# Kernel optimization log

Measured on AMD Instinct MI355X. Metric: run time of the kernel, lower is better.

Reference implementation:

```python
import jax, jax.numpy as jnp
import numpy as np

B, L, D, H = 4, 2048, 1024, 8
DH = D // H
NEG = float(-2**32 + 1)  # padding value used by the torch module


def setup_inputs() -> dict:
    key = jax.random.key(0)
    ks = jax.random.split(key, 7)
    queries = jax.random.normal(ks[0], (B, L, D), dtype=jnp.float32)
    keys = jax.random.normal(ks[1], (B, L, D), dtype=jnp.float32)
    sequence_length = jax.random.randint(ks[2], (B,), 1, L + 1, dtype=jnp.int32)
    scale = 0.02
    W_q = jax.random.normal(ks[3], (D, D), dtype=jnp.float32) * scale
    W_k = jax.random.normal(ks[4], (D, D), dtype=jnp.float32) * scale
    W_v = jax.random.normal(ks[5], (D, D), dtype=jnp.float32) * scale
    W_o = jax.random.normal(ks[6], (D, D), dtype=jnp.float32) * scale
    return {"queries": queries, "keys": keys, "sequence_length": sequence_length,
            "W_q": W_q, "W_k": W_k, "W_v": W_v, "W_o": W_o}


def reference(queries, keys, sequence_length, W_q, W_k, W_v, W_o):
    b, lq, d = queries.shape
    lk = keys.shape[1]
    # projections (nn.Linear, no bias): x @ W.T
    Q = (queries @ W_q.T).reshape(b, lq, H, DH).transpose(2, 0, 1, 3)  # (H,B,Lq,dh)
    K = (keys @ W_k.T).reshape(b, lk, H, DH).transpose(2, 0, 1, 3)
    V = (keys @ W_v.T).reshape(b, lk, H, DH).transpose(2, 0, 1, 3)
    scores = jnp.einsum('hbqd,hbkd->hbqk', Q, K) / jnp.sqrt(jnp.float32(DH))
    # additive key mask: positions >= sequence_length get large negative
    key_mask = jnp.arange(lk)[None, :] < sequence_length[:, None]      # (B,Lk)
    scores = jnp.where(key_mask[None, :, None, :], scores, NEG)
    attn = jax.nn.softmax(scores, axis=-1)
    # post-softmax multiplicative query mask
    q_mask = (jnp.arange(lq)[None, :] < sequence_length[:, None]).astype(attn.dtype)  # (B,Lq)
    attn = attn * q_mask[None, :, :, None]
    out = jnp.einsum('hbqk,hbkd->hbqd', attn, V)                       # (H,B,Lq,dh)
    # chunk-cat order: head h occupies columns h*dh:(h+1)*dh
    out = out.transpose(1, 2, 0, 3).reshape(b, lq, d)
    return out @ W_o.T  # dropout_rate=0 -> identity
```

## Files before the change

kernel.cpp:

```cpp
#include <hip/hip_runtime.h>
#include <math.h>

constexpr int Bsz = 4;
constexpr int Lsz = 2048;
constexpr int Dsz = 1024;
constexpr int Hn  = 8;
constexpr int Dh  = 128;
constexpr int GM  = Bsz * Lsz;
constexpr int GK  = Dsz;
constexpr int NT  = GK / 32;

typedef __attribute__((ext_vector_type(8))) short bf16x8;
typedef __attribute__((ext_vector_type(4))) float f32x4;

union FragU { unsigned int u[4]; bf16x8 f; };

__device__ __forceinline__ void gload16(const void* g, void* l) {
    __builtin_amdgcn_global_load_lds(
        (const __attribute__((address_space(1))) unsigned int*)g,
        (__attribute__((address_space(3))) unsigned int*)l, 16, 0, 0);
}

__device__ __forceinline__ void split2(float f0, float f1,
                                       unsigned int& hp, unsigned int& lp) {
    unsigned int u0 = __float_as_uint(f0), u1 = __float_as_uint(f1);
    hp = (u0 >> 16) | (u1 & 0xffff0000u);
    float l0 = f0 - __uint_as_float(u0 & 0xffff0000u);
    float l1 = f1 - __uint_as_float(u1 & 0xffff0000u);
    lp = (__float_as_uint(l0) >> 16) | (__float_as_uint(l1) & 0xffff0000u);
}

__device__ __forceinline__ void split4(float4 f, ushort4& h, ushort4& l2) {
    unsigned int ux = __float_as_uint(f.x), uy = __float_as_uint(f.y),
                 uz = __float_as_uint(f.z), uw = __float_as_uint(f.w);
    h.x = (unsigned short)(ux >> 16); h.y = (unsigned short)(uy >> 16);
    h.z = (unsigned short)(uz >> 16); h.w = (unsigned short)(uw >> 16);
    float lx = f.x - __uint_as_float(ux & 0xffff0000u);
    float ly = f.y - __uint_as_float(uy & 0xffff0000u);
    float lz = f.z - __uint_as_float(uz & 0xffff0000u);
    float lw = f.w - __uint_as_float(uw & 0xffff0000u);
    l2.x = (unsigned short)(__float_as_uint(lx) >> 16);
    l2.y = (unsigned short)(__float_as_uint(ly) >> 16);
    l2.z = (unsigned short)(__float_as_uint(lz) >> 16);
    l2.w = (unsigned short)(__float_as_uint(lw) >> 16);
}

struct WConv4 {
    const float4* w[4];
    ushort4* h[4];
    ushort4* l[4];
    float s[4];
};

__global__ __launch_bounds__(256) void conv_w4(WConv4 a) {
    int wi = blockIdx.x >> 10;
    int i = (blockIdx.x & 1023) * 256 + threadIdx.x;
    float4 f = a.w[wi][i];
    float s = a.s[wi];
    f.x *= s; f.y *= s; f.z *= s; f.w *= s;
    ushort4 h, l;
    split4(f, h, l);
    a.h[wi][i] = h; a.l[wi][i] = l;
}

__device__ __forceinline__ void compute_tile(const ushort* Ah, const ushort* Al,
                                             const ushort* Bh, const ushort* Bl,
                                             int wm, int wn, int l,
                                             f32x4 acc[2][4]) {
    bf16x8 bh[4], bl4[4], ah[2], al[2];
#pragma unroll
    for (int fn = 0; fn < 4; ++fn) {
        int fng = wn * 4 + fn;
        bh[fn]  = *(const bf16x8*)&Bh[(fng * 64 + l) * 8];
        bl4[fn] = *(const bf16x8*)&Bl[(fng * 64 + l) * 8];
    }
#pragma unroll
    for (int fm = 0; fm < 2; ++fm) {
        int fmg = wm * 2 + fm;
        ah[fm] = *(const bf16x8*)&Ah[(fmg * 64 + l) * 8];
        al[fm] = *(const bf16x8*)&Al[(fmg * 64 + l) * 8];
    }
    __builtin_amdgcn_s_setprio(1);
#pragma unroll
    for (int fm = 0; fm < 2; ++fm)
#pragma unroll
        for (int fn = 0; fn < 4; ++fn) {
            acc[fm][fn] = __builtin_amdgcn_mfma_f32_16x16x32_bf16(
                ah[fm], bh[fn], acc[fm][fn], 0, 0, 0);
            acc[fm][fn] = __builtin_amdgcn_mfma_f32_16x16x32_bf16(
                ah[fm], bl4[fn], acc[fm][fn], 0, 0, 0);
            acc[fm][fn] = __builtin_amdgcn_mfma_f32_16x16x32_bf16(
                al[fm], bh[fn], acc[fm][fn], 0, 0, 0);
        }
    __builtin_amdgcn_s_setprio(0);
}

__device__ __forceinline__ void split_write(ushort* Ah, ushort* Al, int aw,
                                            float4 v0, float4 v1) {
    uint4 h4, l4;
    split2(v0.x, v0.y, h4.x, l4.x);
    split2(v0.z, v0.w, h4.y, l4.y);
    split2(v1.x, v1.y, h4.z, l4.z);
    split2(v1.z, v1.w, h4.w, l4.w);
    *(uint4*)&Ah[aw] = h4;
    *(uint4*)&Al[aw] = l4;
}

__global__ __launch_bounds__(512, 2) void gemm_qkv(
    const float* __restrict__ Aq, const float* __restrict__ Ak,
    const ushort* __restrict__ Wfh, const ushort* __restrict__ Wfl,
    ushort* __restrict__ Qhi, ushort* __restrict__ Qlo,
    ushort* __restrict__ Khi, ushort* __restrict__ Klo,
    ushort* __restrict__ Vthi, ushort* __restrict__ Vtlo,
    const int* __restrict__ slen)
{
    const int tid = threadIdx.x;
    const int bm = blockIdx.y << 7;
    const int bn = blockIdx.x << 7;
    const int grp = bn >> 10;

    const int nk = slen[bm >> 11];
    if ((bm & (Lsz - 1)) >= nk) return;

    __shared__ __align__(16) ushort lds[2][4][128 * 32];

    const float* A = (grp == 0) ? Aq : Ak;
    const int w  = tid >> 6;
    const int l  = tid & 63;
    const int wm = w >> 1;
    const int wn = w & 1;

    const int arow = tid >> 2;
    const int akk  = (tid & 3) << 3;
    const float* ag = A + (size_t)(bm + arow) * GK + akk;
    const int aw = ((((arow >> 4) << 6) + ((akk >> 3) << 4) + (arow & 15)) << 3);

    const int brow = ((tid >> 6) << 4) + (tid & 15);
    const int bkk  = ((tid >> 4) & 3) << 3;
    const ushort* bgh = Wfh + (size_t)(bn + brow) * GK + bkk;
    const ushort* bgl = Wfl + (size_t)(bn + brow) * GK + bkk;

    f32x4 acc[2][4];
#pragma unroll
    for (int i = 0; i < 2; ++i)
#pragma unroll
        for (int j = 0; j < 4; ++j) acc[i][j] = (f32x4)0.f;

    {
        float4 tC0 = *(const float4*)(ag);
        float4 tC1 = *(const float4*)(ag + 4);
        gload16(bgh, &lds[0][2][tid * 8]);
        gload16(bgl, &lds[0][3][tid * 8]);
        split_write(&lds[0][0][0], &lds[0][1][0], aw, tC0, tC1);
    }
    float4 rN0 = *(const float4*)(ag + 32);
    float4 rN1 = *(const float4*)(ag + 36);
    float4 rA0, rA1;
    __syncthreads();

    for (int t = 0; t < NT - 2; t += 2) {
        rA0 = *(const float4*)(ag + (t + 2) * 32);
        rA1 = *(const float4*)(ag + (t + 2) * 32 + 4);
        gload16(bgh + (t + 1) * 32, &lds[1][2][tid * 8]);
        gload16(bgl + (t + 1) * 32, &lds[1][3][tid * 8]);
        split_write(&lds[1][0][0], &lds[1][1][0], aw, rN0, rN1);
        compute_tile(&lds[0][0][0], &lds[0][1][0], &lds[0][2][0], &lds[0][3][0],
                     wm, wn, l, acc);
        __syncthreads();

        rN0 = *(const float4*)(ag + (t + 3) * 32);
        rN1 = *(const float4*)(ag + (t + 3) * 32 + 4);
        gload16(bgh + (t + 2) * 32, &lds[0][2][tid * 8]);
        gload16(bgl + (t + 2) * 32, &lds[0][3][tid * 8]);
        split_write(&lds[0][0][0], &lds[0][1][0], aw, rA0, rA1);
        compute_tile(&lds[1][0][0], &lds[1][1][0], &lds[1][2][0], &lds[1][3][0],
                     wm, wn, l, acc);
        __syncthreads();
    }

    gload16(bgh + (NT - 1) * 32, &lds[1][2][tid * 8]);
    gload16(bgl + (NT - 1) * 32, &lds[1][3][tid * 8]);
    split_write(&lds[1][0][0], &lds[1][1][0], aw, rN0, rN1);
    compute_tile(&lds[0][0][0], &lds[0][1][0], &lds[0][2][0], &lds[0][3][0],
                 wm, wn, l, acc);
    __syncthreads();

    compute_tile(&lds[1][0][0], &lds[1][1][0], &lds[1][2][0], &lds[1][3][0],
                 wm, wn, l, acc);

    const int rq = (l >> 4) << 2;
    const int cq = l & 15;
    ushort* OH = (grp == 0) ? Qhi : Khi;
    ushort* OL = (grp == 0) ? Qlo : Klo;
#pragma unroll
    for (int fm = 0; fm < 2; ++fm) {
        int r0 = bm + wm * 32 + fm * 16 + rq;
#pragma unroll
        for (int fn = 0; fn < 4; ++fn) {
            int cn = (bn & 1023) + wn * 64 + fn * 16 + cq;
            if (grp < 2) {
#pragma unroll
                for (int r = 0; r < 4; ++r) {
                    float f = acc[fm][fn][r];
                    unsigned int u = __float_as_uint(f);
                    float res = f - __uint_as_float(u & 0xffff0000u);
                    OH[(size_t)(r0 + r) * Dsz + cn] = (unsigned short)(u >> 16);
                    OL[(size_t)(r0 + r) * Dsz + cn] =
                        (unsigned short)(__float_as_uint(res) >> 16);
                }
            } else {
                ushort4 h4, l4;
                unsigned short* hp = (unsigned short*)&h4;
                unsigned short* lp = (unsigned short*)&l4;
#pragma unroll
                for (int r = 0; r < 4; ++r) {
                    float f = acc[fm][fn][r];
                    unsigned int u = __float_as_uint(f);
                    float res = f - __uint_as_float(u & 0xffff0000u);
                    hp[r] = (unsigned short)(u >> 16);
                    lp[r] = (unsigned short)(__float_as_uint(res) >> 16);
                }
                *(ushort4*)&Vthi[(size_t)cn * GM + r0] = h4;
                *(ushort4*)&Vtlo[(size_t)cn * GM + r0] = l4;
            }
        }
    }
}

__global__ __launch_bounds__(512, 2) void gemm_o(
    const ushort* __restrict__ Ahi, const ushort* __restrict__ Alo,
    const ushort* __restrict__ Bhi, const ushort* __restrict__ Blo,
    float* __restrict__ C, const int* __restrict__ slen)
{
    const int tid = threadIdx.x;
    const int bm = blockIdx.y << 7;
    const int bn = blockIdx.x << 7;

    const int nk = slen[bm >> 11];
    if ((bm & (Lsz - 1)) >= nk) {
        int row = tid >> 2;
        int cb  = (tid & 3) << 5;
        float4 z = make_float4(0.f, 0.f, 0.f, 0.f);
        float4* cp = (float4*)(C + (size_t)(bm + row) * Dsz + bn + cb);
#pragma unroll
        for (int i = 0; i < 8; ++i) cp[i] = z;
        return;
    }

    __shared__ __align__(16) ushort lds[2][4][128 * 32];

    const int w  = tid >> 6;
    const int l  = tid & 63;
    const int wm = w >> 1;
    const int wn = w & 1;

    const int srow = ((tid >> 6) << 4) + (tid & 15);
    const int skk  = ((tid >> 4) & 3) << 3;
    const ushort* agh = Ahi + (size_t)(bm + srow) * GK + skk;
    const ushort* agl = Alo + (size_t)(bm + srow) * GK + skk;
    const ushort* bgh = Bhi + (size_t)(bn + srow) * GK + skk;
    const ushort* bgl = Blo + (size_t)(bn + srow) * GK + skk;

    f32x4 acc[2][4];
#pragma unroll
    for (int i = 0; i < 2; ++i)
#pragma unroll
        for (int j = 0; j < 4; ++j) acc[i][j] = (f32x4)0.f;

    gload16(agh, &lds[0][0][tid * 8]);
    gload16(agl, &lds[0][1][tid * 8]);
    gload16(bgh, &lds[0][2][tid * 8]);
    gload16(bgl, &lds[0][3][tid * 8]);
    __syncthreads();

    for (int t = 0; t < NT - 1; ++t) {
        const int p = t & 1;
        const int q = p ^ 1;
        gload16(agh + (t + 1) * 32, &lds[q][0][tid * 8]);
        gload16(agl + (t + 1) * 32, &lds[q][1][tid * 8]);
        gload16(bgh + (t + 1) * 32, &lds[q][2][tid * 8]);
        gload16(bgl + (t + 1) * 32, &lds[q][3][tid * 8]);
        compute_tile(&lds[p][0][0], &lds[p][1][0], &lds[p][2][0], &lds[p][3][0],
                     wm, wn, l, acc);
        __syncthreads();
    }
    {
        const int p = (NT - 1) & 1;
        compute_tile(&lds[p][0][0], &lds[p][1][0], &lds[p][2][0], &lds[p][3][0],
                     wm, wn, l, acc);
    }

    const int rq = (l >> 4) << 2;
    const int cq = l & 15;
#pragma unroll
    for (int fm = 0; fm < 2; ++fm) {
        int r0 = bm + wm * 32 + fm * 16 + rq;
#pragma unroll
        for (int fn = 0; fn < 4; ++fn) {
            int c0 = bn + wn * 64 + fn * 16 + cq;
#pragma unroll
            for (int r = 0; r < 4; ++r)
                C[(size_t)(r0 + r) * Dsz + c0] = acc[fm][fn][r];
        }
    }
}

__global__ __launch_bounds__(512) void flash_mfma(
    const ushort* __restrict__ Qhi, const ushort* __restrict__ Qlo,
    const ushort* __restrict__ Khi, const ushort* __restrict__ Klo,
    const ushort* __restrict__ Vthi, const ushort* __restrict__ Vtlo,
    const int* __restrict__ slen,
    ushort* __restrict__ Ohi, ushort* __restrict__ Olo)
{
    __shared__ __align__(16) ushort Ks[32 * 256];
    __shared__ __align__(16) ushort Vs[128 * 64];
    __shared__ __align__(16) unsigned int Pb[8 * 16 * 36];

    const int tid = threadIdx.x;
    const int w = tid >> 6, l = tid & 63;
    const int lg = l >> 4, lc = l & 15;
    const int q0 = blockIdx.x << 7;
    const int h = blockIdx.y, b = blockIdx.z;
    const int nk = slen[b];

    if (q0 >= nk) return;

    bf16x8 qh[4], ql[4];
    {
        size_t base = (size_t)(b * Lsz + q0 + (w << 4) + lc) * Dsz + h * Dh + lg * 8;
#pragma unroll
        for (int s = 0; s < 4; ++s) {
            qh[s] = *(const bf16x8*)&Qhi[base + s * 32];
            ql[s] = *(const bf16x8*)&Qlo[base + s * 32];
        }
    }

    const ushort* ksrc[2]; int klds[2];
    const ushort* vsrc[2]; int vlds[2];
#pragma unroll
    for (int i = 0; i < 2; ++i) {
        int s = i * 512 + tid;
        int j = s >> 5, p = s & 31;
        int lg4 = (p & 15) ^ (j & 15);
        const ushort* base = (p & 16) ? Klo : Khi;
        ksrc[i] = base + (size_t)(b * Lsz + j) * Dsz + h * Dh + lg4 * 8;
        klds[i] = s * 8;
    }
#pragma unroll
    for (int i = 0; i < 2; ++i) {
        int s = i * 512 + tid;
        int d = s >> 3, p = s & 7;
        int lgc = p ^ (d & 7);
        const ushort* base = (lgc & 4) ? Vtlo : Vthi;
        vsrc[i] = base + (size_t)(h * Dh + d) * (Bsz * Lsz) + b * Lsz + (lgc & 3) * 8;
        vlds[i] = s * 8;
    }

    f32x4 oacc[8];
#pragma unroll
    for (int fd = 0; fd < 8; ++fd) oacc[fd] = (f32x4)0.f;
    float lsum[4] = {0.f, 0.f, 0.f, 0.f};
    const int pbase = w * (16 * 36);

    for (int kb = 0; kb < nk; kb += 32) {
#pragma unroll
        for (int i = 0; i < 2; ++i) gload16(ksrc[i] + (size_t)kb * Dsz, &Ks[klds[i]]);
#pragma unroll
        for (int i = 0; i < 2; ++i) gload16(vsrc[i] + kb, &Vs[vlds[i]]);
        __syncthreads();

        f32x4 sa[2] = {(f32x4)0.f, (f32x4)0.f};
#pragma unroll
        for (int fn = 0; fn < 2; ++fn) {
            int j = fn * 16 + lc;
            int ro = j * 256;
#pragma unroll
            for (int s = 0; s < 4; ++s) {
                int phys = (s * 4 + lg) ^ (j & 15);
                bf16x8 kh = *(const bf16x8*)&Ks[ro + phys * 8];
                bf16x8 kl = *(const bf16x8*)&Ks[ro + 128 + phys * 8];
                sa[fn] = __builtin_amdgcn_mfma_f32_16x16x32_bf16(qh[s], kh, sa[fn], 0, 0, 0);
                sa[fn] = __builtin_amdgcn_mfma_f32_16x16x32_bf16(qh[s], kl, sa[fn], 0, 0, 0);
                sa[fn] = __builtin_amdgcn_mfma_f32_16x16x32_bf16(ql[s], kh, sa[fn], 0, 0, 0);
            }
        }

        if (kb + 32 > nk) {
#pragma unroll
            for (int fn = 0; fn < 2; ++fn) {
                bool oob = (kb + fn * 16 + lc) >= nk;
#pragma unroll
                for (int rr = 0; rr < 4; ++rr)
                    sa[fn][rr] = oob ? -1e30f : sa[fn][rr];
            }
        }

#pragma unroll
        for (int fn = 0; fn < 2; ++fn)
#pragma unroll
            for (int rr = 0; rr < 4; ++rr) {
                float p = __expf(sa[fn][rr]);
                lsum[rr] += p;
                unsigned int u = __float_as_uint(p);
                float res = p - __uint_as_float(u & 0xffff0000u);
                unsigned int lo16 = __float_as_uint(res) >> 16;
                Pb[pbase + (lg * 4 + rr) * 36 + fn * 16 + lc] =
                    (lo16 << 16) | (u >> 16);
            }

        const unsigned int* pr = &Pb[pbase + lc * 36 + lg * 8];
        uint4 a0 = *(const uint4*)pr;
        uint4 a1 = *(const uint4*)(pr + 4);
        FragU PH, PL;
        PH.u[0] = (a0.x & 0xffffu) | (a0.y << 16);
        PH.u[1] = (a0.z & 0xffffu) | (a0.w << 16);
        PH.u[2] = (a1.x & 0xffffu) | (a1.y << 16);
        PH.u[3] = (a1.z & 0xffffu) | (a1.w << 16);
        PL.u[0] = (a0.x >> 16) | (a0.y & 0xffff0000u);
        PL.u[1] = (a0.z >> 16) | (a0.w & 0xffff0000u);
        PL.u[2] = (a1.x >> 16) | (a1.y & 0xffff0000u);
        PL.u[3] = (a1.z >> 16) | (a1.w & 0xffff0000u);

#pragma unroll
        for (int fd = 0; fd < 8; ++fd) {
            int d = fd * 16 + lc;
            int ro = d * 64;
            int ph = lg ^ (d & 7);
            int pl2 = (4 + lg) ^ (d & 7);
            bf16x8 vh = *(const bf16x8*)&Vs[ro + ph * 8];
            bf16x8 vl = *(const bf16x8*)&Vs[ro + pl2 * 8];
            oacc[fd] = __builtin_amdgcn_mfma_f32_16x16x32_bf16(PH.f, vh, oacc[fd], 0, 0, 0);
            oacc[fd] = __builtin_amdgcn_mfma_f32_16x16x32_bf16(PH.f, vl, oacc[fd], 0, 0, 0);
            oacc[fd] = __builtin_amdgcn_mfma_f32_16x16x32_bf16(PL.f, vh, oacc[fd], 0, 0, 0);
        }
        __syncthreads();
    }

#pragma unroll
    for (int m = 1; m < 16; m <<= 1)
#pragma unroll
        for (int rr = 0; rr < 4; ++rr)
            lsum[rr] += __shfl_xor(lsum[rr], m, 64);

#pragma unroll
    for (int rr = 0; rr < 4; ++rr) {
        int q = q0 + (w << 4) + (lg << 2) + rr;
        bool valid = q < nk;
        float inv = valid ? (1.f / lsum[rr]) : 0.f;
        size_t base = (size_t)(b * Lsz + q) * Dsz + h * Dh + lc;
#pragma unroll
        for (int fd = 0; fd < 8; ++fd) {
            float val = valid ? oacc[fd][rr] * inv : 0.f;
            unsigned int u = __float_as_uint(val);
            float res = val - __uint_as_float(u & 0xffff0000u);
            Ohi[base + fd * 16] = (unsigned short)(u >> 16);
            Olo[base + fd * 16] = (unsigned short)(__float_as_uint(res) >> 16);
        }
    }
}

extern "C" void kernel_launch(void* const* d_in, const int* in_sizes, int n_in,
                              void* d_out, int out_size, void* d_ws, size_t ws_size,
                              hipStream_t stream) {
    (void)in_sizes; (void)n_in; (void)out_size; (void)ws_size;
    const float* queries = (const float*)d_in[0];
    const float* keys    = (const float*)d_in[1];
    const int*   slen    = (const int*)d_in[2];
    const float* Wq      = (const float*)d_in[3];
    const float* Wk      = (const float*)d_in[4];
    const float* Wv      = (const float*)d_in[5];
    const float* Wo      = (const float*)d_in[6];
    float* out = (float*)d_out;

    const size_t MD = (size_t)Bsz * Lsz * Dsz;
    const size_t WD = (size_t)Dsz * Dsz;
    ushort* Qhi  = (ushort*)d_ws;
    ushort* Qlo  = Qhi + MD;
    ushort* Khi  = Qlo + MD;
    ushort* Klo  = Khi + MD;
    ushort* Vthi = Klo + MD;
    ushort* Vtlo = Vthi + MD;
    ushort* Wfh  = Vtlo + MD;
    ushort* Wfl  = Wfh + 3 * WD;
    ushort* Woh  = Wfl + 3 * WD;
    ushort* Wol  = Woh + WD;

    const float scaleQ = 0.08838834764831845f;
    WConv4 wa;
    wa.w[0] = (const float4*)Wq; wa.h[0] = (ushort4*)Wfh;            wa.l[0] = (ushort4*)Wfl;            wa.s[0] = scaleQ;
    wa.w[1] = (const float4*)Wk; wa.h[1] = (ushort4*)(Wfh + WD);     wa.l[1] = (ushort4*)(Wfl + WD);     wa.s[1] = 1.f;
    wa.w[2] = (const float4*)Wv; wa.h[2] = (ushort4*)(Wfh + 2 * WD); wa.l[2] = (ushort4*)(Wfl + 2 * WD); wa.s[2] = 1.f;
    wa.w[3] = (const float4*)Wo; wa.h[3] = (ushort4*)Woh;            wa.l[3] = (ushort4*)Wol;            wa.s[3] = 1.f;
    conv_w4<<<4096, 256, 0, stream>>>(wa);

    gemm_qkv<<<dim3(24, 64), 512, 0, stream>>>(
        queries, keys, Wfh, Wfl, Qhi, Qlo, Khi, Klo, Vthi, Vtlo, slen);

    dim3 ga(Lsz / 128, Hn, Bsz);
    flash_mfma<<<ga, 512, 0, stream>>>(Qhi, Qlo, Khi, Klo, Vthi, Vtlo, slen,
                                       Qhi, Qlo );

    gemm_o<<<dim3(8, 64), 512, 0, stream>>>(Qhi, Qlo, Woh, Wol, out, slen);
}
```

Before: 395.0 us.

## Use partial vmcnt waits and XOR-swizzle A tile LDS layout in GEMMs

The GEMM main loops now wait for only the older global-to-LDS loads (vmcnt 4/2/0) before a raw barrier, instead of a full __syncthreads, so the next tile's loads stay in flight while the current tile computes. The QKV GEMM also XOR-swizzles the row index of the A tile in LDS to reduce bank conflicts on the split-bf16 writes and reads. The hand-written waitcnt values depend on exact instruction counts and could race if the compiler emits a different number of memory operations.

```diff
diff --git a/kernel.cpp b/kernel.cpp
--- a/kernel.cpp
+++ b/kernel.cpp
@@ -65,7 +65,7 @@
 
 __device__ __forceinline__ void compute_tile(const ushort* Ah, const ushort* Al,
                                              const ushort* Bh, const ushort* Bl,
-                                             int wm, int wn, int l,
+                                             int wm, int wn, int l, int la,
                                              f32x4 acc[2][4]) {
     bf16x8 bh[4], bl4[4], ah[2], al[2];
 #pragma unroll
@@ -77,8 +77,8 @@
 #pragma unroll
     for (int fm = 0; fm < 2; ++fm) {
         int fmg = wm * 2 + fm;
-        ah[fm] = *(const bf16x8*)&Ah[(fmg * 64 + l) * 8];
-        al[fm] = *(const bf16x8*)&Al[(fmg * 64 + l) * 8];
+        ah[fm] = *(const bf16x8*)&Ah[(fmg * 64 + la) * 8];
+        al[fm] = *(const bf16x8*)&Al[(fmg * 64 + la) * 8];
     }
     __builtin_amdgcn_s_setprio(1);
 #pragma unroll
@@ -105,6 +105,19 @@
     *(uint4*)&Ah[aw] = h4;
     *(uint4*)&Al[aw] = l4;
 }
+
+#define FRONT_WAIT_4()  do { \
+    asm volatile("s_waitcnt vmcnt(4) lgkmcnt(0)" ::: "memory"); \
+    __builtin_amdgcn_sched_barrier(0); \
+    __builtin_amdgcn_s_barrier(); } while (0)
+#define FRONT_WAIT_2()  do { \
+    asm volatile("s_waitcnt vmcnt(2) lgkmcnt(0)" ::: "memory"); \
+    __builtin_amdgcn_sched_barrier(0); \
+    __builtin_amdgcn_s_barrier(); } while (0)
+#define FRONT_WAIT_0()  do { \
+    asm volatile("s_waitcnt vmcnt(0) lgkmcnt(0)" ::: "memory"); \
+    __builtin_amdgcn_sched_barrier(0); \
+    __builtin_amdgcn_s_barrier(); } while (0)
 
 __global__ __launch_bounds__(512, 2) void gemm_qkv(
     const float* __restrict__ Aq, const float* __restrict__ Ak,
@@ -129,11 +142,12 @@
     const int l  = tid & 63;
     const int wm = w >> 1;
     const int wn = w & 1;
+    const int la = l ^ ((l >> 4) << 1);
 
     const int arow = tid >> 2;
-    const int akk  = (tid & 3) << 3;
-    const float* ag = A + (size_t)(bm + arow) * GK + akk;
-    const int aw = ((((arow >> 4) << 6) + ((akk >> 3) << 4) + (arow & 15)) << 3);
+    const int kg   = tid & 3;
+    const float* ag = A + (size_t)(bm + arow) * GK + (kg << 3);
+    const int aw = ((((arow >> 4) << 6) + (kg << 4) + ((arow & 15) ^ (kg << 1))) << 3);
 
     const int brow = ((tid >> 6) << 4) + (tid & 15);
     const int bkk  = ((tid >> 4) & 3) << 3;
@@ -146,47 +160,48 @@
 #pragma unroll
         for (int j = 0; j < 4; ++j) acc[i][j] = (f32x4)0.f;
 
-    {
-        float4 tC0 = *(const float4*)(ag);
-        float4 tC1 = *(const float4*)(ag + 4);
-        gload16(bgh, &lds[0][2][tid * 8]);
-        gload16(bgl, &lds[0][3][tid * 8]);
-        split_write(&lds[0][0][0], &lds[0][1][0], aw, tC0, tC1);
-    }
-    float4 rN0 = *(const float4*)(ag + 32);
-    float4 rN1 = *(const float4*)(ag + 36);
-    float4 rA0, rA1;
-    __syncthreads();
+    float4 pA0 = *(const float4*)(ag);
+    float4 pA1 = *(const float4*)(ag + 4);
+    gload16(bgh, &lds[0][2][tid * 8]);
+    gload16(bgl, &lds[0][3][tid * 8]);
+    float4 rA0 = *(const float4*)(ag + 32);
+    float4 rA1 = *(const float4*)(ag + 36);
+    float4 rB0, rB1;
+    split_write(&lds[0][0][0], &lds[0][1][0], aw, pA0, pA1);
 
     for (int t = 0; t < NT - 2; t += 2) {
-        rA0 = *(const float4*)(ag + (t + 2) * 32);
-        rA1 = *(const float4*)(ag + (t + 2) * 32 + 4);
+        rB0 = *(const float4*)(ag + (t + 2) * 32);
+        rB1 = *(const float4*)(ag + (t + 2) * 32 + 4);
         gload16(bgh + (t + 1) * 32, &lds[1][2][tid * 8]);
         gload16(bgl + (t + 1) * 32, &lds[1][3][tid * 8]);
-        split_write(&lds[1][0][0], &lds[1][1][0], aw, rN0, rN1);
+        split_write(&lds[1][0][0], &lds[1][1][0], aw, rA0, rA1);
+        FRONT_WAIT_4();
         compute_tile(&lds[0][0][0], &lds[0][1][0], &lds[0][2][0], &lds[0][3][0],
-                     wm, wn, l, acc);
-        __syncthreads();
-
-        rN0 = *(const float4*)(ag + (t + 3) * 32);
-        rN1 = *(const float4*)(ag + (t + 3) * 32 + 4);
+                     wm, wn, l, la, acc);
+        __builtin_amdgcn_s_barrier();
+
+        rA0 = *(const float4*)(ag + (t + 3) * 32);
+        rA1 = *(const float4*)(ag + (t + 3) * 32 + 4);
         gload16(bgh + (t + 2) * 32, &lds[0][2][tid * 8]);
         gload16(bgl + (t + 2) * 32, &lds[0][3][tid * 8]);
-        split_write(&lds[0][0][0], &lds[0][1][0], aw, rA0, rA1);
+        split_write(&lds[0][0][0], &lds[0][1][0], aw, rB0, rB1);
+        FRONT_WAIT_4();
         compute_tile(&lds[1][0][0], &lds[1][1][0], &lds[1][2][0], &lds[1][3][0],
-                     wm, wn, l, acc);
-        __syncthreads();
+                     wm, wn, l, la, acc);
+        __builtin_amdgcn_s_barrier();
     }
 
     gload16(bgh + (NT - 1) * 32, &lds[1][2][tid * 8]);
     gload16(bgl + (NT - 1) * 32, &lds[1][3][tid * 8]);
-    split_write(&lds[1][0][0], &lds[1][1][0], aw, rN0, rN1);
+    split_write(&lds[1][0][0], &lds[1][1][0], aw, rA0, rA1);
+    FRONT_WAIT_2();
     compute_tile(&lds[0][0][0], &lds[0][1][0], &lds[0][2][0], &lds[0][3][0],
-                 wm, wn, l, acc);
-    __syncthreads();
-
+                 wm, wn, l, la, acc);
+    __builtin_amdgcn_s_barrier();
+
+    FRONT_WAIT_0();
     compute_tile(&lds[1][0][0], &lds[1][1][0], &lds[1][2][0], &lds[1][3][0],
-                 wm, wn, l, acc);
+                 wm, wn, l, la, acc);
 
     const int rq = (l >> 4) << 2;
     const int cq = l & 15;
@@ -267,28 +282,35 @@
 #pragma unroll
         for (int j = 0; j < 4; ++j) acc[i][j] = (f32x4)0.f;
 
-    gload16(agh, &lds[0][0][tid * 8]);
-    gload16(agl, &lds[0][1][tid * 8]);
-    gload16(bgh, &lds[0][2][tid * 8]);
-    gload16(bgl, &lds[0][3][tid * 8]);
-    __syncthreads();
-
-    for (int t = 0; t < NT - 1; ++t) {
-        const int p = t & 1;
-        const int q = p ^ 1;
-        gload16(agh + (t + 1) * 32, &lds[q][0][tid * 8]);
-        gload16(agl + (t + 1) * 32, &lds[q][1][tid * 8]);
-        gload16(bgh + (t + 1) * 32, &lds[q][2][tid * 8]);
-        gload16(bgl + (t + 1) * 32, &lds[q][3][tid * 8]);
-        compute_tile(&lds[p][0][0], &lds[p][1][0], &lds[p][2][0], &lds[p][3][0],
-                     wm, wn, l, acc);
-        __syncthreads();
-    }
-    {
-        const int p = (NT - 1) & 1;
-        compute_tile(&lds[p][0][0], &lds[p][1][0], &lds[p][2][0], &lds[p][3][0],
-                     wm, wn, l, acc);
-    }
+#define STAGE_O(tt, bb) do { \
+    gload16(agh + (tt) * 32, &lds[bb][0][tid * 8]); \
+    gload16(agl + (tt) * 32, &lds[bb][1][tid * 8]); \
+    gload16(bgh + (tt) * 32, &lds[bb][2][tid * 8]); \
+    gload16(bgl + (tt) * 32, &lds[bb][3][tid * 8]); } while (0)
+
+    STAGE_O(0, 0);
+
+    for (int t = 0; t < NT - 2; t += 2) {
+        STAGE_O(t + 1, 1);
+        FRONT_WAIT_4();
+        compute_tile(&lds[0][0][0], &lds[0][1][0], &lds[0][2][0], &lds[0][3][0],
+                     wm, wn, l, l, acc);
+        __builtin_amdgcn_s_barrier();
+        STAGE_O(t + 2, 0);
+        FRONT_WAIT_4();
+        compute_tile(&lds[1][0][0], &lds[1][1][0], &lds[1][2][0], &lds[1][3][0],
+                     wm, wn, l, l, acc);
+        __builtin_amdgcn_s_barrier();
+    }
+    STAGE_O(NT - 1, 1);
+    FRONT_WAIT_4();
+    compute_tile(&lds[0][0][0], &lds[0][1][0], &lds[0][2][0], &lds[0][3][0],
+                 wm, wn, l, l, acc);
+    __builtin_amdgcn_s_barrier();
+    FRONT_WAIT_0();
+    compute_tile(&lds[1][0][0], &lds[1][1][0], &lds[1][2][0], &lds[1][3][0],
+                 wm, wn, l, l, acc);
+#undef STAGE_O
 
     const int rq = (l >> 4) << 2;
     const int cq = l & 15;
```

New measurement: 399.8 us. Within noise of the previous version (+1.2%).

## Load A fragments directly into registers, stage only B through LDS in projection GEMMs

Applied to the files above, without the earlier changes.

In both the QKV and output projection GEMMs, the A operand is now read from global memory straight into each wave's MFMA fragment registers, with the hi/lo bf16 split done in registers, rather than being staged through shared memory. Only the weight (B) tiles keep going through double-buffered LDS, so the LDS footprint halves and launch bounds rise to allow more resident blocks. The aim is to cut LDS writes, LDS reads and footprint per block. The cost is that each wave re-reads its A rows from global memory, because waves sharing the same rows no longer share them through LDS.

```diff
diff --git a/kernel.cpp b/kernel.cpp
--- a/kernel.cpp
+++ b/kernel.cpp
@@ -28,6 +28,13 @@
     float l0 = f0 - __uint_as_float(u0 & 0xffff0000u);
     float l1 = f1 - __uint_as_float(u1 & 0xffff0000u);
     lp = (__float_as_uint(l0) >> 16) | (__float_as_uint(l1) & 0xffff0000u);
+}
+
+__device__ __forceinline__ void splitA(float4 f0, float4 f1, FragU& h, FragU& lo) {
+    split2(f0.x, f0.y, h.u[0], lo.u[0]);
+    split2(f0.z, f0.w, h.u[1], lo.u[1]);
+    split2(f1.x, f1.y, h.u[2], lo.u[2]);
+    split2(f1.z, f1.w, h.u[3], lo.u[3]);
 }
 
 __device__ __forceinline__ void split4(float4 f, ushort4& h, ushort4& l2) {
@@ -63,50 +70,31 @@
     a.h[wi][i] = h; a.l[wi][i] = l;
 }
 
-__device__ __forceinline__ void compute_tile(const ushort* Ah, const ushort* Al,
+__device__ __forceinline__ void mfma_cluster(bf16x8 a0h, bf16x8 a0l,
+                                             bf16x8 a1h, bf16x8 a1l,
                                              const ushort* Bh, const ushort* Bl,
-                                             int wm, int wn, int l,
-                                             f32x4 acc[2][4]) {
-    bf16x8 bh[4], bl4[4], ah[2], al[2];
+                                             int wn, int l, f32x4 acc[2][4]) {
+    bf16x8 bh[4], bl4[4];
 #pragma unroll
     for (int fn = 0; fn < 4; ++fn) {
         int fng = wn * 4 + fn;
         bh[fn]  = *(const bf16x8*)&Bh[(fng * 64 + l) * 8];
         bl4[fn] = *(const bf16x8*)&Bl[(fng * 64 + l) * 8];
     }
-#pragma unroll
-    for (int fm = 0; fm < 2; ++fm) {
-        int fmg = wm * 2 + fm;
-        ah[fm] = *(const bf16x8*)&Ah[(fmg * 64 + l) * 8];
-        al[fm] = *(const bf16x8*)&Al[(fmg * 64 + l) * 8];
-    }
     __builtin_amdgcn_s_setprio(1);
 #pragma unroll
-    for (int fm = 0; fm < 2; ++fm)
-#pragma unroll
-        for (int fn = 0; fn < 4; ++fn) {
-            acc[fm][fn] = __builtin_amdgcn_mfma_f32_16x16x32_bf16(
-                ah[fm], bh[fn], acc[fm][fn], 0, 0, 0);
-            acc[fm][fn] = __builtin_amdgcn_mfma_f32_16x16x32_bf16(
-                ah[fm], bl4[fn], acc[fm][fn], 0, 0, 0);
-            acc[fm][fn] = __builtin_amdgcn_mfma_f32_16x16x32_bf16(
-                al[fm], bh[fn], acc[fm][fn], 0, 0, 0);
-        }
+    for (int fn = 0; fn < 4; ++fn) {
+        acc[0][fn] = __builtin_amdgcn_mfma_f32_16x16x32_bf16(a0h, bh[fn],  acc[0][fn], 0, 0, 0);
+        acc[0][fn] = __builtin_amdgcn_mfma_f32_16x16x32_bf16(a0h, bl4[fn], acc[0][fn], 0, 0, 0);
+        acc[0][fn] = __builtin_amdgcn_mfma_f32_16x16x32_bf16(a0l, bh[fn],  acc[0][fn], 0, 0, 0);
+        acc[1][fn] = __builtin_amdgcn_mfma_f32_16x16x32_bf16(a1h, bh[fn],  acc[1][fn], 0, 0, 0);
+        acc[1][fn] = __builtin_amdgcn_mfma_f32_16x16x32_bf16(a1h, bl4[fn], acc[1][fn], 0, 0, 0);
+        acc[1][fn] = __builtin_amdgcn_mfma_f32_16x16x32_bf16(a1l, bh[fn],  acc[1][fn], 0, 0, 0);
+    }
     __builtin_amdgcn_s_setprio(0);
 }
 
-__device__ __forceinline__ void split_write(ushort* Ah, ushort* Al, int aw,
-                                            float4 v0, float4 v1) {
-    uint4 h4, l4;
-    split2(v0.x, v0.y, h4.x, l4.x);
-    split2(v0.z, v0.w, h4.y, l4.y);
-    split2(v1.x, v1.y, h4.z, l4.z);
-    split2(v1.z, v1.w, h4.w, l4.w);
-    *(uint4*)&Ah[aw] = h4;
-    *(uint4*)&Al[aw] = l4;
-}
-
-__global__ __launch_bounds__(512, 2) void gemm_qkv(
+__global__ __launch_bounds__(512, 4) void gemm_qkv(
     const float* __restrict__ Aq, const float* __restrict__ Ak,
     const ushort* __restrict__ Wfh, const ushort* __restrict__ Wfl,
     ushort* __restrict__ Qhi, ushort* __restrict__ Qlo,
@@ -122,18 +110,17 @@
     const int nk = slen[bm >> 11];
     if ((bm & (Lsz - 1)) >= nk) return;
 
-    __shared__ __align__(16) ushort lds[2][4][128 * 32];
+    __shared__ __align__(16) ushort Bs[2][2][128 * 32];
 
     const float* A = (grp == 0) ? Aq : Ak;
     const int w  = tid >> 6;
     const int l  = tid & 63;
     const int wm = w >> 1;
     const int wn = w & 1;
-
-    const int arow = tid >> 2;
-    const int akk  = (tid & 3) << 3;
-    const float* ag = A + (size_t)(bm + arow) * GK + akk;
-    const int aw = ((((arow >> 4) << 6) + ((akk >> 3) << 4) + (arow & 15)) << 3);
+    const int lg = l >> 4, lc = l & 15;
+
+    const float* agA0 = A + (size_t)(bm + wm * 32 +  0 + lc) * GK + lg * 8;
+    const float* agA1 = A + (size_t)(bm + wm * 32 + 16 + lc) * GK + lg * 8;
 
     const int brow = ((tid >> 6) << 4) + (tid & 15);
     const int bkk  = ((tid >> 4) & 3) << 3;
@@ -146,47 +133,68 @@
 #pragma unroll
         for (int j = 0; j < 4; ++j) acc[i][j] = (f32x4)0.f;
 
+    float4 c00 = *(const float4*)(agA0);
+    float4 c01 = *(const float4*)(agA0 + 4);
+    float4 c10 = *(const float4*)(agA1);
+    float4 c11 = *(const float4*)(agA1 + 4);
+    gload16(bgh, &Bs[0][0][tid * 8]);
+    gload16(bgl, &Bs[0][1][tid * 8]);
+    float4 n00 = *(const float4*)(agA0 + 32);
+    float4 n01 = *(const float4*)(agA0 + 36);
+    float4 n10 = *(const float4*)(agA1 + 32);
+    float4 n11 = *(const float4*)(agA1 + 36);
+    __syncthreads();
+
+    for (int t = 0; t < NT - 2; t += 2) {
+        gload16(bgh + (t + 1) * 32, &Bs[1][0][tid * 8]);
+        gload16(bgl + (t + 1) * 32, &Bs[1][1][tid * 8]);
+        {
+            FragU a0h, a0l, a1h, a1l;
+            splitA(c00, c01, a0h, a0l);
+            splitA(c10, c11, a1h, a1l);
+            c00 = *(const float4*)(agA0 + (t + 2) * 32);
+            c01 = *(const float4*)(agA0 + (t + 2) * 32 + 4);
+            c10 = *(const float4*)(agA1 + (t + 2) * 32);
+            c11 = *(const float4*)(agA1 + (t + 2) * 32 + 4);
+            mfma_cluster(a0h.f, a0l.f, a1h.f, a1l.f,
+                         &Bs[0][0][0], &Bs[0][1][0], wn, l, acc);
+        }
+        __syncthreads();
+
+        gload16(bgh + (t + 2) * 32, &Bs[0][0][tid * 8]);
+        gload16(bgl + (t + 2) * 32, &Bs[0][1][tid * 8]);
+        {
+            FragU a0h, a0l, a1h, a1l;
+            splitA(n00, n01, a0h, a0l);
+            splitA(n10, n11, a1h, a1l);
+            n00 = *(const float4*)(agA0 + (t + 3) * 32);
+            n01 = *(const float4*)(agA0 + (t + 3) * 32 + 4);
+            n10 = *(const float4*)(agA1 + (t + 3) * 32);
+            n11 = *(const float4*)(agA1 + (t + 3) * 32 + 4);
+            mfma_cluster(a0h.f, a0l.f, a1h.f, a1l.f,
+                         &Bs[1][0][0], &Bs[1][1][0], wn, l, acc);
+        }
+        __syncthreads();
+    }
+
+    gload16(bgh + (NT - 1) * 32, &Bs[1][0][tid * 8]);
+    gload16(bgl + (NT - 1) * 32, &Bs[1][1][tid * 8]);
     {
-        float4 tC0 = *(const float4*)(ag);
-        float4 tC1 = *(const float4*)(ag + 4);
-        gload16(bgh, &lds[0][2][tid * 8]);
-        gload16(bgl, &lds[0][3][tid * 8]);
-        split_write(&lds[0][0][0], &lds[0][1][0], aw, tC0, tC1);
-    }
-    float4 rN0 = *(const float4*)(ag + 32);
-    float4 rN1 = *(const float4*)(ag + 36);
-    float4 rA0, rA1;
+        FragU a0h, a0l, a1h, a1l;
+        splitA(c00, c01, a0h, a0l);
+        splitA(c10, c11, a1h, a1l);
+        mfma_cluster(a0h.f, a0l.f, a1h.f, a1l.f,
+                     &Bs[0][0][0], &Bs[0][1][0], wn, l, acc);
+    }
     __syncthreads();
 
-    for (int t = 0; t < NT - 2; t += 2) {
-        rA0 = *(const float4*)(ag + (t + 2) * 32);
-        rA1 = *(const float4*)(ag + (t + 2) * 32 + 4);
-        gload16(bgh + (t + 1) * 32, &lds[1][2][tid * 8]);
-        gload16(bgl + (t + 1) * 32, &lds[1][3][tid * 8]);
-        split_write(&lds[1][0][0], &lds[1][1][0], aw, rN0, rN1);
-        compute_tile(&lds[0][0][0], &lds[0][1][0], &lds[0][2][0], &lds[0][3][0],
-                     wm, wn, l, acc);
-        __syncthreads();
-
-        rN0 = *(const float4*)(ag + (t + 3) * 32);
-        rN1 = *(const float4*)(ag + (t + 3) * 32 + 4);
-        gload16(bgh + (t + 2) * 32, &lds[0][2][tid * 8]);
-        gload16(bgl + (t + 2) * 32, &lds[0][3][tid * 8]);
-        split_write(&lds[0][0][0], &lds[0][1][0], aw, rA0, rA1);
-        compute_tile(&lds[1][0][0], &lds[1][1][0], &lds[1][2][0], &lds[1][3][0],
-                     wm, wn, l, acc);
-        __syncthreads();
-    }
-
-    gload16(bgh + (NT - 1) * 32, &lds[1][2][tid * 8]);
-    gload16(bgl + (NT - 1) * 32, &lds[1][3][tid * 8]);
-    split_write(&lds[1][0][0], &lds[1][1][0], aw, rN0, rN1);
-    compute_tile(&lds[0][0][0], &lds[0][1][0], &lds[0][2][0], &lds[0][3][0],
-                 wm, wn, l, acc);
-    __syncthreads();
-
-    compute_tile(&lds[1][0][0], &lds[1][1][0], &lds[1][2][0], &lds[1][3][0],
-                 wm, wn, l, acc);
+    {
+        FragU a0h, a0l, a1h, a1l;
+        splitA(n00, n01, a0h, a0l);
+        splitA(n10, n11, a1h, a1l);
+        mfma_cluster(a0h.f, a0l.f, a1h.f, a1l.f,
+                     &Bs[1][0][0], &Bs[1][1][0], wn, l, acc);
+    }
 
     const int rq = (l >> 4) << 2;
     const int cq = l & 15;
@@ -227,7 +235,7 @@
     }
 }
 
-__global__ __launch_bounds__(512, 2) void gemm_o(
+__global__ __launch_bounds__(512, 4) void gemm_o(
     const ushort* __restrict__ Ahi, const ushort* __restrict__ Alo,
     const ushort* __restrict__ Bhi, const ushort* __restrict__ Blo,
     float* __restrict__ C, const int* __restrict__ slen)
@@ -247,17 +255,21 @@
         return;
     }
 
-    __shared__ __align__(16) ushort lds[2][4][128 * 32];
+    __shared__ __align__(16) ushort Bs[2][2][128 * 32];
 
     const int w  = tid >> 6;
     const int l  = tid & 63;
     const int wm = w >> 1;
     const int wn = w & 1;
+    const int lg = l >> 4, lc = l & 15;
+
+    const ushort* a0hP = Ahi + (size_t)(bm + wm * 32 +  0 + lc) * GK + lg * 8;
+    const ushort* a0lP = Alo + (size_t)(bm + wm * 32 +  0 + lc) * GK + lg * 8;
+    const ushort* a1hP = Ahi + (size_t)(bm + wm * 32 + 16 + lc) * GK + lg * 8;
+    const ushort* a1lP = Alo + (size_t)(bm + wm * 32 + 16 + lc) * GK + lg * 8;
 
     const int srow = ((tid >> 6) << 4) + (tid & 15);
     const int skk  = ((tid >> 4) & 3) << 3;
-    const ushort* agh = Ahi + (size_t)(bm + srow) * GK + skk;
-    const ushort* agl = Alo + (size_t)(bm + srow) * GK + skk;
     const ushort* bgh = Bhi + (size_t)(bn + srow) * GK + skk;
     const ushort* bgl = Blo + (size_t)(bn + srow) * GK + skk;
 
@@ -267,28 +279,46 @@
 #pragma unroll
         for (int j = 0; j < 4; ++j) acc[i][j] = (f32x4)0.f;
 
-    gload16(agh, &lds[0][0][tid * 8]);
-    gload16(agl, &lds[0][1][tid * 8]);
-    gload16(bgh, &lds[0][2][tid * 8]);
-    gload16(bgl, &lds[0][3][tid * 8]);
+    bf16x8 c0h = *(const bf16x8*)(a0hP), c0l = *(const bf16x8*)(a0lP);
+    bf16x8 c1h = *(const bf16x8*)(a1hP), c1l = *(const bf16x8*)(a1lP);
+    gload16(bgh, &Bs[0][0][tid * 8]);
+    gload16(bgl, &Bs[0][1][tid * 8]);
+    bf16x8 n0h = *(const bf16x8*)(a0hP + 32), n0l = *(const bf16x8*)(a0lP + 32);
+    bf16x8 n1h = *(const bf16x8*)(a1hP + 32), n1l = *(const bf16x8*)(a1lP + 32);
     __syncthreads();
 
-    for (int t = 0; t < NT - 1; ++t) {
-        const int p = t & 1;
-        const int q = p ^ 1;
-        gload16(agh + (t + 1) * 32, &lds[q][0][tid * 8]);
-        gload16(agl + (t + 1) * 32, &lds[q][1][tid * 8]);
-        gload16(bgh + (t + 1) * 32, &lds[q][2][tid * 8]);
-        gload16(bgl + (t + 1) * 32, &lds[q][3][tid * 8]);
-        compute_tile(&lds[p][0][0], &lds[p][1][0], &lds[p][2][0], &lds[p][3][0],
-                     wm, wn, l, acc);
+    for (int t = 0; t < NT - 2; t += 2) {
+        gload16(bgh + (t + 1) * 32, &Bs[1][0][tid * 8]);
+        gload16(bgl + (t + 1) * 32, &Bs[1][1][tid * 8]);
+        {
+            bf16x8 a0h = c0h, a0l = c0l, a1h = c1h, a1l = c1l;
+            c0h = *(const bf16x8*)(a0hP + (t + 2) * 32);
+            c0l = *(const bf16x8*)(a0lP + (t + 2) * 32);
+            c1h = *(const bf16x8*)(a1hP + (t + 2) * 32);
+            c1l = *(const bf16x8*)(a1lP + (t + 2) * 32);
+            mfma_cluster(a0h, a0l, a1h, a1l,
+                         &Bs[0][0][0], &Bs[0][1][0], wn, l, acc);
+        }
         __syncthreads();
-    }
-    {
-        const int p = (NT - 1) & 1;
-        compute_tile(&lds[p][0][0], &lds[p][1][0], &lds[p][2][0], &lds[p][3][0],
-                     wm, wn, l, acc);
-    }
+
+        gload16(bgh + (t + 2) * 32, &Bs[0][0][tid * 8]);
+        gload16(bgl + (t + 2) * 32, &Bs[0][1][tid * 8]);
+        {
+            bf16x8 a0h = n0h, a0l = n0l, a1h = n1h, a1l = n1l;
+            n0h = *(const bf16x8*)(a0hP + (t + 3) * 32);
+            n0l = *(const bf16x8*)(a0lP + (t + 3) * 32);
+            n1h = *(const bf16x8*)(a1hP + (t + 3) * 32);
+            n1l = *(const bf16x8*)(a1lP + (t + 3) * 32);
+            mfma_cluster(a0h, a0l, a1h, a1l,
+                         &Bs[1][0][0], &Bs[1][1][0], wn, l, acc);
+        }
+        __syncthreads();
+    }
+    gload16(bgh + (NT - 1) * 32, &Bs[1][0][tid * 8]);
+    gload16(bgl + (NT - 1) * 32, &Bs[1][1][tid * 8]);
+    mfma_cluster(c0h, c0l, c1h, c1l, &Bs[0][0][0], &Bs[0][1][0], wn, l, acc);
+    __syncthreads();
+    mfma_cluster(n0h, n0l, n1h, n1l, &Bs[1][0][0], &Bs[1][1][0], wn, l, acc);
 
     const int rq = (l >> 4) << 2;
     const int cq = l & 15;
```

New measurement: 547.9 us. 1.39x slower.
